# Kernel tuning notes

Hardware: AMD Instinct MI355X
Metric: run time of the kernel (lower is better)

## Reference

```python
import jax, jax.numpy as jnp
import numpy as np

STRIDES = [(2, 2), (3, 3), (4, 4)]
EPS = 1e-5


def _conv1x1(x, w, b):
    # x: [B,C,H,W], w: [O,C] -> [B,O,H,W]
    return jnp.einsum('bchw,oc->bohw', x, w) + b[None, :, None, None]


def _stitch(x, hs, ws):
    # x: [B,dk,H,W] -> patches [B, hs*ws, dk*oh*ow]; patch index = i*ws + j matches
    # torch.stack over itertools.product(range(hs), range(ws)) of x[:,:,i::hs,j::ws]
    b, dk, H, W = x.shape
    oh, ow = H // hs, W // ws
    p = x.reshape(b, dk, oh, hs, ow, ws).transpose(0, 3, 5, 1, 2, 4)  # [B,hs,ws,dk,oh,ow]
    return p.reshape(b, hs * ws, dk * oh * ow)


def _unstitch(y, b, dk, hs, ws, oh, ow):
    # faithful to the torch permute(0,3,1,4,2,5): H is assembled as (hs, oh), W as (ws, ow)
    y = y.reshape(b, hs, ws, dk, oh, ow).transpose(0, 3, 1, 4, 2, 5)  # [B,dk,hs,oh,ws,ow]
    return y.reshape(b, dk, hs * oh, ws * ow)


def _attention(q, k, v):
    d = q.shape[-1]
    scores = jnp.einsum('bpd,bqd->bpq', q, k) / jnp.sqrt(jnp.asarray(d, q.dtype))
    p = jax.nn.softmax(scores, axis=-1)
    return jnp.einsum('bpq,bqd->bpd', p, v)


def _forward(x, wq, bq, wk, bk, wv, bv, w_out, b_out, gamma, beta):
    b, c, h, w = x.shape
    n = len(STRIDES)
    dk = c // n
    q = _conv1x1(x, wq, bq)
    k = _conv1x1(x, wk, bk)
    v = _conv1x1(x, wv, bv)
    outs = []
    for idx, (ws_, hs_) in enumerate(STRIDES):
        sl = slice(idx * dk, (idx + 1) * dk)
        oh, ow = h // hs_, w // ws_
        qp = _stitch(q[:, sl], hs_, ws_)
        kp = _stitch(k[:, sl], hs_, ws_)
        vp = _stitch(v[:, sl], hs_, ws_)
        y = _attention(qp, kp, vp)  # [B, hs*ws, dk*oh*ow]
        outs.append(_unstitch(y, b, dk, hs_, ws_, oh, ow))
    out = jnp.concatenate(outs, axis=1)  # [B,C,H,W]
    # output_linear: Conv3x3 -> BatchNorm2d (training-mode batch stats) -> LeakyReLU(0.2)
    y = jax.lax.conv_general_dilated(out, w_out, (1, 1), 'SAME',
                                     dimension_numbers=('NCHW', 'OIHW', 'NCHW'))
    y = y + b_out[None, :, None, None]
    mean = jnp.mean(y, axis=(0, 2, 3), keepdims=True)
    var = jnp.var(y, axis=(0, 2, 3), keepdims=True)
    y = (y - mean) * jax.lax.rsqrt(var + EPS)
    y = y * gamma[None, :, None, None] + beta[None, :, None, None]
    return jnp.where(y >= 0, y, 0.2 * y)


def setup_inputs() -> dict:
    key = jax.random.key(0)
    ks = jax.random.split(key, 10)
    B, C, H, W = 16, 192, 96, 96
    s = 0.02
    return {
        'x': jax.random.normal(ks[0], (B, C, H, W), jnp.float32),
        'wq': jax.random.normal(ks[1], (C, C), jnp.float32) * s,
        'bq': jnp.zeros((C,), jnp.float32),
        'wk': jax.random.normal(ks[2], (C, C), jnp.float32) * s,
        'bk': jnp.zeros((C,), jnp.float32),
        'wv': jax.random.normal(ks[3], (C, C), jnp.float32) * s,
        'bv': jnp.zeros((C,), jnp.float32),
        'w_out': jax.random.normal(ks[4], (C, C, 3, 3), jnp.float32) * s,
        'b_out': jnp.zeros((C,), jnp.float32),
        'gamma': jnp.ones((C,), jnp.float32),
        'beta': jnp.zeros((C,), jnp.float32),
    }


def reference(x, wq, bq, wk, bk, wv, bv, w_out, b_out, gamma, beta):
    return _forward(x, wq, bq, wk, bk, wv, bv, w_out, b_out, gamma, beta)
```

## Files before the change

### kernel.cpp

```cpp
#include <hip/hip_runtime.h>
#include <hip/hip_bf16.h>

#define BB 16
#define CC 192
#define HH 96
#define WWW 96
#define HWSZ 9216
#define DKC 64

typedef __hip_bfloat16 bf16;
typedef __attribute__((ext_vector_type(8))) short s8v;
typedef __attribute__((ext_vector_type(4))) float f32x4;

__device__ __forceinline__ float bf2f(unsigned short u) {
  union { unsigned int i; float f; } x; x.i = ((unsigned int)u) << 16; return x.f;
}
__device__ __forceinline__ unsigned short f2bf(float f) {
  union { __hip_bfloat16 h; unsigned short u; } c; c.h = __float2bfloat16(f); return c.u;
}

__global__ __launch_bounds__(256) void prep_w_kernel(const float* __restrict__ w_out,
                                                     unsigned short* __restrict__ wb9T) {
  int e = blockIdx.x * 256 + threadIdx.x;
  if (e >= 9 * CC * CC) return;
  int c = e % CC;
  int oc = (e / CC) % CC;
  int sh = e / (CC * CC);
  wb9T[e] = f2bf(w_out[((size_t)(oc * CC + c)) * 9 + sh]);
}

__global__ __launch_bounds__(256) void prep_wqkv_kernel(
    const float* __restrict__ wq, const float* __restrict__ wk, const float* __restrict__ wv,
    unsigned short* __restrict__ wqkv) {
  int e = blockIdx.x * 256 + threadIdx.x;
  if (e >= 3 * CC * CC) return;
  int sel = e / (CC * CC), r = e % (CC * CC);
  const float* w = sel == 0 ? wq : sel == 1 ? wk : wv;
  wqkv[e] = f2bf(w[r]);
}

__global__ __launch_bounds__(256) void xcvt_kernel(const float* __restrict__ x,
                                                   unsigned short* __restrict__ xb) {
  __shared__ float xt[CC][65];
  int b = blockIdx.x / 144, tile = blockIdx.x % 144;
  int pix0 = tile * 64;
  const float* xsrc = x + (size_t)b * CC * HWSZ + pix0;
  for (int e = threadIdx.x; e < CC * 16; e += 256) {
    int c = e >> 4, seg = e & 15;
    float4 t4 = *(const float4*)(xsrc + (size_t)c * HWSZ + seg * 4);
    xt[c][seg * 4 + 0] = t4.x; xt[c][seg * 4 + 1] = t4.y;
    xt[c][seg * 4 + 2] = t4.z; xt[c][seg * 4 + 3] = t4.w;
  }
  __syncthreads();
  unsigned short* dst = xb + ((size_t)(b * HWSZ + pix0)) * CC;
  for (int e = threadIdx.x; e < 24 * 64; e += 256) {
    int cg = e >> 6, p = e & 63;
    uint4 ov;
    unsigned short* ou = (unsigned short*)&ov;
    #pragma unroll
    for (int j = 0; j < 8; ++j) ou[j] = f2bf(xt[cg * 8 + j][p]);
    *(uint4*)(dst + (size_t)p * CC + cg * 8) = ov;
  }
}

__global__ __launch_bounds__(256) void qkv_mfma_kernel(
    const unsigned short* __restrict__ xb, const unsigned short* __restrict__ wqkv,
    const float* __restrict__ bq, const float* __restrict__ bk, const float* __restrict__ bv,
    unsigned short* __restrict__ q, unsigned short* __restrict__ k,
    unsigned short* __restrict__ v) {
  __shared__ unsigned short al[2][96 * 40];
  __shared__ unsigned short vt[48 * 224];
  const int tid = threadIdx.x;
  const int bid = (blockIdx.x & 7) * 576 + (blockIdx.x >> 3);
  const int sel = bid % 3;
  const int h = (bid / 3) % HH;
  const int b = bid / (3 * HH);
  const int lane = tid & 63, wid = tid >> 6;
  const int lr = lane & 15, hi8 = (lane >> 4) * 8, rowb = (lane >> 4) * 4;
  const int n0 = wid * 48;
  const unsigned short* xrow = xb + ((size_t)(b * HWSZ + h * WWW)) * CC;
  const unsigned short* wsel = wqkv + (size_t)sel * CC * CC;

  f32x4 acc[6][3];
  #pragma unroll
  for (int mt = 0; mt < 6; ++mt)
    #pragma unroll
    for (int nt = 0; nt < 3; ++nt) acc[mt][nt] = (f32x4){0.f, 0.f, 0.f, 0.f};

  auto loadB = [&](int ck, s8v (&dst)[3]) {
    const unsigned short* src = wsel + ck * 32 + hi8;
    #pragma unroll
    for (int nt = 0; nt < 3; ++nt)
      dst[nt] = *(const s8v*)(src + (size_t)(n0 + nt * 16 + lr) * CC);
  };

  s8v br0[3], br1[3], br2[3];
  {
    uint4 a0 = *(const uint4*)(xrow + (size_t)(tid >> 2) * CC + (tid & 3) * 8);
    uint4 a1;
    int u1 = tid + 256;
    if (u1 < 384) a1 = *(const uint4*)(xrow + (size_t)(u1 >> 2) * CC + (u1 & 3) * 8);
    loadB(0, br0); loadB(1, br1); loadB(2, br2);
    *(uint4*)(al[0] + (tid >> 2) * 40 + (tid & 3) * 8) = a0;
    if (u1 < 384) *(uint4*)(al[0] + (u1 >> 2) * 40 + (u1 & 3) * 8) = a1;
  }
  __syncthreads();

  auto qstep = [&](int ck, s8v (&slot)[3]) {
    uint4 ar0, ar1;
    int u1 = tid + 256;
    if (ck < 5) {
      ar0 = *(const uint4*)(xrow + (size_t)(tid >> 2) * CC + (ck + 1) * 32 + (tid & 3) * 8);
      if (u1 < 384)
        ar1 = *(const uint4*)(xrow + (size_t)(u1 >> 2) * CC + (ck + 1) * 32 + (u1 & 3) * 8);
    }
    const unsigned short* A = al[ck & 1];
    s8v a[6];
    #pragma unroll
    for (int mt = 0; mt < 6; ++mt)
      a[mt] = *(const s8v*)(A + (mt * 16 + lr) * 40 + hi8);
    #pragma unroll
    for (int mt = 0; mt < 6; ++mt)
      #pragma unroll
      for (int nt = 0; nt < 3; ++nt)
        acc[mt][nt] = __builtin_amdgcn_mfma_f32_16x16x32_bf16(a[mt], slot[nt], acc[mt][nt], 0, 0, 0);
    if (ck + 3 < 6) loadB(ck + 3, slot);
    if (ck < 5) {
      unsigned short* dstA = al[(ck + 1) & 1];
      *(uint4*)(dstA + (tid >> 2) * 40 + (tid & 3) * 8) = ar0;
      if (u1 < 384) *(uint4*)(dstA + (u1 >> 2) * 40 + (u1 & 3) * 8) = ar1;
    }
    __syncthreads();
  };
  qstep(0, br0); qstep(1, br1); qstep(2, br2);
  qstep(3, br0); qstep(4, br1); qstep(5, br2);

  const float* bsel = (sel == 0 ? bq : sel == 1 ? bk : bv);
  float bias[3];
  #pragma unroll
  for (int nt = 0; nt < 3; ++nt) bias[nt] = bsel[n0 + nt * 16 + lr];
  unsigned short* dst = (sel == 0 ? q : sel == 1 ? k : v) + ((size_t)(b * HWSZ + h * WWW)) * CC;
  #pragma unroll
  for (int pass = 0; pass < 2; ++pass) {
    if (pass) __syncthreads();
    #pragma unroll
    for (int mt2 = 0; mt2 < 3; ++mt2) {
      #pragma unroll
      for (int nt = 0; nt < 3; ++nt)
        #pragma unroll
        for (int i = 0; i < 4; ++i)
          vt[(mt2 * 16 + rowb + i) * 224 + n0 + nt * 16 + lr] =
              f2bf(acc[pass * 3 + mt2][nt][i] + bias[nt]);
    }
    __syncthreads();
    for (int e = tid; e < 48 * 24; e += 256) {
      int p = e % 48, cg = e / 48;
      *(uint4*)(dst + (size_t)(pass * 48 + p) * CC + cg * 8) = *(uint4*)(vt + p * 224 + cg * 8);
    }
  }
}

template <int HS, int WS, int OH, int OW, int IDX>
__global__ __launch_bounds__(256) void scores_kernel(
    const unsigned short* __restrict__ q, const unsigned short* __restrict__ k,
    float* __restrict__ scores) {
  constexpr int P = HS * WS;
  constexpr int PAIRS = P * P;
  constexpr int NB = 16;
  constexpr int NSUB = (256 / PAIRS) < 1 ? 1 : (256 / PAIRS);
  __shared__ float qt[128][P + 1];
  __shared__ float kt[128][P + 1];
  int b = blockIdx.x / NB;
  int blk = blockIdx.x % NB;
  const unsigned short* qb = q + (size_t)b * HWSZ * CC;
  const unsigned short* kb = k + (size_t)b * HWSZ * CC;
  int pr = threadIdx.x % PAIRS;
  int sub = threadIdx.x / PAIRS;
  int pi = pr / P, qi = pr % P;
  float acc = 0.f;
  for (int rs0 = blk * 2; rs0 < OH * OW; rs0 += NB * 2) {
    if (threadIdx.x < 16 * P) {
      int cg = threadIdx.x & 7;
      int t2 = threadIdx.x >> 3;
      int pp = t2 % P, rs2 = t2 / P;
      int rs = rs0 + rs2;
      int r = rs / OW, s = rs % OW;
      int i = pp / WS, j = pp % WS;
      int pixel = (r * HS + i) * WWW + s * WS + j;
      uint4 qv = *(const uint4*)(qb + (size_t)pixel * CC + IDX * 64 + cg * 8);
      uint4 kv = *(const uint4*)(kb + (size_t)pixel * CC + IDX * 64 + cg * 8);
      const unsigned short* qu = (const unsigned short*)&qv;
      const unsigned short* ku = (const unsigned short*)&kv;
      #pragma unroll
      for (int m = 0; m < 8; ++m) {
        qt[rs2 * 64 + cg * 8 + m][pp] = bf2f(qu[m]);
        kt[rs2 * 64 + cg * 8 + m][pp] = bf2f(ku[m]);
      }
    }
    __syncthreads();
    if (sub < NSUB) {
      #pragma unroll 4
      for (int pos = sub; pos < 128; pos += NSUB)
        acc += qt[pos][pi] * kt[pos][qi];
    }
    __syncthreads();
  }
  if (sub < NSUB) atomicAdd(scores + ((IDX * BB + b) * 256 + pr), acc);
}

__global__ void softmax_kernel(const float* __restrict__ scores, float* __restrict__ probs) {
  int t = threadIdx.x;
  int idx, b, p, P; float scale;
  if (t < 64)       { idx = 0; b = t >> 2;           p = t & 3;         P = 4;  scale = 1.f / 384.f; }
  else if (t < 208) { int u = t - 64;  idx = 1; b = u / 9;  p = u % 9;  P = 9;  scale = 1.f / 256.f; }
  else if (t < 464) { int u = t - 208; idx = 2; b = u >> 4; p = u & 15; P = 16; scale = 1.f / 192.f; }
  else return;
  const float* row = scores + (idx * BB + b) * 256 + p * P;
  float* orow = probs + (idx * BB + b) * 256 + p * P;
  float vals[16];
  float m = -1e30f;
  for (int i = 0; i < P; i++) { vals[i] = row[i] * scale; m = fmaxf(m, vals[i]); }
  float s = 0.f;
  for (int i = 0; i < P; i++) { vals[i] = expf(vals[i] - m); s += vals[i]; }
  float inv = 1.f / s;
  for (int i = 0; i < P; i++) orow[i] = vals[i] * inv;
}

template <int HS, int WS, int OH, int OW, int IDX>
__global__ __launch_bounds__(256) void pv_kernel(
    const unsigned short* __restrict__ v, const float* __restrict__ probs,
    unsigned short* __restrict__ attn) {
  constexpr int P = HS * WS;
  __shared__ unsigned short vl[HS * 96 * 72];
  __shared__ float pl[P * P];
  int b = blockIdx.x / OH;
  int r = blockIdx.x % OH;
  const int tid = threadIdx.x;
  for (int u = tid; u < HS * 96 * 8; u += 256) {
    int iq = u / 768, w = (u >> 3) % 96, cg = u & 7;
    *(uint4*)(vl + (iq * 96 + w) * 72 + cg * 8) =
        *(const uint4*)(v + ((size_t)(b * HWSZ + (r * HS + iq) * WWW + w)) * CC + IDX * 64 + cg * 8);
  }
  if (tid < P * P) pl[tid] = probs[(IDX * BB + b) * 256 + tid];
  __syncthreads();
  for (int u = tid; u < HS * 96 * 8; u += 256) {
    int i = u / 768, w = (u >> 3) % 96, cg = u & 7;
    int j = w / OW, s = w - j * OW;
    int p = i * WS + j;
    float acc[8];
    #pragma unroll
    for (int m = 0; m < 8; ++m) acc[m] = 0.f;
    #pragma unroll
    for (int iq = 0; iq < HS; ++iq) {
      #pragma unroll
      for (int jq = 0; jq < WS; ++jq) {
        float pw = pl[p * P + iq * WS + jq];
        s8v vv = *(const s8v*)(vl + (iq * 96 + s * WS + jq) * 72 + cg * 8);
        #pragma unroll
        for (int m = 0; m < 8; ++m) acc[m] += pw * bf2f((unsigned short)vv[m]);
      }
    }
    uint4 ov;
    ov.x = (unsigned int)f2bf(acc[0]) | ((unsigned int)f2bf(acc[1]) << 16);
    ov.y = (unsigned int)f2bf(acc[2]) | ((unsigned int)f2bf(acc[3]) << 16);
    ov.z = (unsigned int)f2bf(acc[4]) | ((unsigned int)f2bf(acc[5]) << 16);
    ov.w = (unsigned int)f2bf(acc[6]) | ((unsigned int)f2bf(acc[7]) << 16);
    *(uint4*)(attn + ((size_t)(b * HWSZ + (i * OH + r) * WWW + w)) * CC + IDX * 64 + cg * 8) = ov;
  }
}

__global__ __launch_bounds__(256) void conv_mfma_kernel(
    const unsigned short* __restrict__ attn, const unsigned short* __restrict__ wb9T,
    const float* __restrict__ b_out, unsigned short* __restrict__ ybf,
    float* __restrict__ bnsum, float* __restrict__ bnsqs) {
  __shared__ unsigned short al[2][3 * 98 * 40];
  const int tid = threadIdx.x;
  const int bid = (blockIdx.x & 7) * 192 + (blockIdx.x >> 3);
  const int h = bid % HH;
  const int b = bid / HH;
  const int lane = tid & 63, wid = tid >> 6;
  const int lr = lane & 15, hi8 = (lane >> 4) * 8, rowb = (lane >> 4) * 4;
  const int n0 = wid * 48;

  f32x4 acc[6][3];
  #pragma unroll
  for (int mt = 0; mt < 6; ++mt)
    #pragma unroll
    for (int nt = 0; nt < 3; ++nt) acc[mt][nt] = (f32x4){0.f, 0.f, 0.f, 0.f};

  uint4 aregs[5];
  auto stageA_LOAD = [&](int chunk) {
    int c0 = chunk * 32;
    #pragma unroll
    for (int i = 0; i < 5; ++i) {
      int u = tid + i * 256;
      if (u < 1176) {
        int row = u / 392, rem = u % 392, wx = rem >> 2, qq = rem & 3;
        int hr = h + row - 1, w = wx - 1;
        uint4 val = make_uint4(0u, 0u, 0u, 0u);
        if (hr >= 0 && hr < HH && w >= 0 && w < WWW)
          val = *(const uint4*)(attn + ((size_t)(b * HWSZ + hr * WWW + w)) * CC + c0 + qq * 8);
        aregs[i] = val;
      }
    }
  };
  auto stageA_WRITE = [&](int chunk) {
    unsigned short* dst = al[chunk & 1];
    #pragma unroll
    for (int i = 0; i < 5; ++i) {
      int u = tid + i * 256;
      if (u < 1176) {
        int row = u / 392, rem = u % 392, wx = rem >> 2, qq = rem & 3;
        *(uint4*)(dst + (row * 98 + wx) * 40 + qq * 8) = aregs[i];
      }
    }
  };
  auto loadB = [&](int it2, s8v (&dst)[3]) {
    int chunk = it2 / 9, sh = it2 % 9;
    const unsigned short* src = wb9T + (size_t)sh * CC * CC + chunk * 32 + hi8;
    #pragma unroll
    for (int nt = 0; nt < 3; ++nt)
      dst[nt] = *(const s8v*)(src + (size_t)(n0 + nt * 16 + lr) * CC);
  };

  s8v br0[3], br1[3], br2[3];
  stageA_LOAD(0);
  stageA_WRITE(0);
  loadB(0, br0); loadB(1, br1); loadB(2, br2);
  __syncthreads();

  auto step = [&](int it, s8v (&slot)[3]) {
    int chunk = it / 9, sh = it % 9, ky = sh / 3, kx = sh % 3;
    if (sh == 0 && chunk < 5) stageA_LOAD(chunk + 1);
    const unsigned short* A = al[chunk & 1];
    s8v a[6];
    #pragma unroll
    for (int mt = 0; mt < 6; ++mt)
      a[mt] = *(const s8v*)(A + (ky * 98 + mt * 16 + lr + kx) * 40 + hi8);
    #pragma unroll
    for (int mt = 0; mt < 6; ++mt)
      #pragma unroll
      for (int nt = 0; nt < 3; ++nt)
        acc[mt][nt] = __builtin_amdgcn_mfma_f32_16x16x32_bf16(a[mt], slot[nt], acc[mt][nt], 0, 0, 0);
    if (it + 3 < 54) loadB(it + 3, slot);
    if (sh == 7 && chunk < 5) stageA_WRITE(chunk + 1);
    if (sh == 8) __syncthreads();
  };
  for (int it3 = 0; it3 < 54; it3 += 3) {
    step(it3 + 0, br0);
    step(it3 + 1, br1);
    step(it3 + 2, br2);
  }

  float s1[3], s2[3];
  #pragma unroll
  for (int nt = 0; nt < 3; ++nt) { s1[nt] = 0.f; s2[nt] = 0.f; }
  #pragma unroll
  for (int nt = 0; nt < 3; ++nt) {
    int oc = n0 + nt * 16 + lr;
    float bias = b_out[oc];
    #pragma unroll
    for (int mt = 0; mt < 6; ++mt) {
      float v0 = acc[mt][nt][0] + bias;
      float v1 = acc[mt][nt][1] + bias;
      float v2 = acc[mt][nt][2] + bias;
      float v3 = acc[mt][nt][3] + bias;
      s1[nt] += v0 + v1 + v2 + v3;
      s2[nt] += v0 * v0 + v1 * v1 + v2 * v2 + v3 * v3;
      uint2 pk;
      pk.x = (unsigned int)f2bf(v0) | ((unsigned int)f2bf(v1) << 16);
      pk.y = (unsigned int)f2bf(v2) | ((unsigned int)f2bf(v3) << 16);
      *(uint2*)(ybf + ((size_t)(b * CC + oc)) * HWSZ + h * WWW + mt * 16 + rowb) = pk;
    }
  }
  #pragma unroll
  for (int nt = 0; nt < 3; ++nt) {
    s1[nt] += __shfl_down(s1[nt], 32);
    s1[nt] += __shfl_down(s1[nt], 16);
    s2[nt] += __shfl_down(s2[nt], 32);
    s2[nt] += __shfl_down(s2[nt], 16);
  }
  if (lane < 16) {
    #pragma unroll
    for (int nt = 0; nt < 3; ++nt) {
      atomicAdd(bnsum + n0 + nt * 16 + lane, s1[nt]);
      atomicAdd(bnsqs + n0 + nt * 16 + lane, s2[nt]);
    }
  }
}

__global__ void bnfin_kernel(const float* __restrict__ bnsum, const float* __restrict__ bnsqs,
                             const float* __restrict__ gamma, const float* __restrict__ beta,
                             float* __restrict__ scale, float* __restrict__ shift) {
  int c = threadIdx.x;
  if (c >= CC) return;
  const float n = 16.f * 9216.f;
  float mean = bnsum[c] / n;
  float var = bnsqs[c] / n - mean * mean;
  float inv = rsqrtf(var + 1e-5f);
  float sc = gamma[c] * inv;
  scale[c] = sc;
  shift[c] = beta[c] - mean * sc;
}

__global__ __launch_bounds__(256) void bnapply_kernel(const unsigned short* __restrict__ ybf,
                                                      float* __restrict__ y,
                                                      const float* __restrict__ scale,
                                                      const float* __restrict__ shift) {
  const int total8 = BB * CC * HWSZ / 8;
  for (int e = blockIdx.x * 256 + threadIdx.x; e < total8; e += gridDim.x * 256) {
    uint4 t = ((const uint4*)ybf)[e];
    const unsigned short* u = (const unsigned short*)&t;
    int oc = (e / (HWSZ / 8)) % CC;
    float sc = scale[oc], sh = shift[oc];
    float4 o0, o1;
    float w;
    w = bf2f(u[0]) * sc + sh; o0.x = w >= 0.f ? w : 0.2f * w;
    w = bf2f(u[1]) * sc + sh; o0.y = w >= 0.f ? w : 0.2f * w;
    w = bf2f(u[2]) * sc + sh; o0.z = w >= 0.f ? w : 0.2f * w;
    w = bf2f(u[3]) * sc + sh; o0.w = w >= 0.f ? w : 0.2f * w;
    w = bf2f(u[4]) * sc + sh; o1.x = w >= 0.f ? w : 0.2f * w;
    w = bf2f(u[5]) * sc + sh; o1.y = w >= 0.f ? w : 0.2f * w;
    w = bf2f(u[6]) * sc + sh; o1.z = w >= 0.f ? w : 0.2f * w;
    w = bf2f(u[7]) * sc + sh; o1.w = w >= 0.f ? w : 0.2f * w;
    ((float4*)y)[e * 2] = o0;
    ((float4*)y)[e * 2 + 1] = o1;
  }
}

extern "C" void kernel_launch(void* const* d_in, const int* in_sizes, int n_in,
                              void* d_out, int out_size, void* d_ws, size_t ws_size,
                              hipStream_t stream) {
  const float* x     = (const float*)d_in[0];
  const float* wq    = (const float*)d_in[1];
  const float* bq    = (const float*)d_in[2];
  const float* wk    = (const float*)d_in[3];
  const float* bk    = (const float*)d_in[4];
  const float* wv    = (const float*)d_in[5];
  const float* bv    = (const float*)d_in[6];
  const float* w_out = (const float*)d_in[7];
  const float* b_out = (const float*)d_in[8];
  const float* gamma = (const float*)d_in[9];
  const float* beta  = (const float*)d_in[10];

  char* ws = (char*)d_ws;
  const size_t TB = (size_t)BB * CC * HWSZ * sizeof(bf16);
  unsigned short* q    = (unsigned short*)(ws);
  unsigned short* ybf  = q;
  unsigned short* k    = (unsigned short*)(ws + TB);
  unsigned short* v    = (unsigned short*)(ws + 2 * TB);
  unsigned short* attn = (unsigned short*)(ws + 3 * TB);
  unsigned short* xb   = attn;
  unsigned short* wb9T = (unsigned short*)(ws + 4 * TB);
  unsigned short* wqkv = (unsigned short*)(ws + 4 * TB + 663552);
  float* scores = (float*)(ws + 4 * TB + 663552 + 221184);
  float* bnsum  = scores + 3 * BB * 256;
  float* bnsqs  = bnsum + CC;
  float* probs  = bnsqs + CC;
  float* scale  = probs + 3 * BB * 256;
  float* shift  = scale + CC;
  float* y = (float*)d_out;

  hipMemsetAsync(scores, 0, 49152 + 2 * CC * 4, stream);

  prep_w_kernel<<<(9 * CC * CC + 255) / 256, 256, 0, stream>>>(w_out, wb9T);
  prep_wqkv_kernel<<<(3 * CC * CC + 255) / 256, 256, 0, stream>>>(wq, wk, wv, wqkv);

  xcvt_kernel<<<BB * 144, 256, 0, stream>>>(x, xb);
  qkv_mfma_kernel<<<BB * HH * 3, 256, 0, stream>>>(xb, wqkv, bq, bk, bv, q, k, v);

  scores_kernel<2, 2, 48, 48, 0><<<BB * 16, 256, 0, stream>>>(q, k, scores);
  scores_kernel<3, 3, 32, 32, 1><<<BB * 16, 256, 0, stream>>>(q, k, scores);
  scores_kernel<4, 4, 24, 24, 2><<<BB * 16, 256, 0, stream>>>(q, k, scores);

  softmax_kernel<<<1, 512, 0, stream>>>(scores, probs);

  pv_kernel<2, 2, 48, 48, 0><<<BB * 48, 256, 0, stream>>>(v, probs, attn);
  pv_kernel<3, 3, 32, 32, 1><<<BB * 32, 256, 0, stream>>>(v, probs, attn);
  pv_kernel<4, 4, 24, 24, 2><<<BB * 24, 256, 0, stream>>>(v, probs, attn);

  conv_mfma_kernel<<<BB * HH, 256, 0, stream>>>(attn, wb9T, b_out, ybf, bnsum, bnsqs);

  bnfin_kernel<<<1, 256, 0, stream>>>(bnsum, bnsqs, gamma, beta, scale, shift);
  bnapply_kernel<<<2048, 256, 0, stream>>>(ybf, y, scale, shift);
}
```

Baseline: 505.4 us.

## Compute Q, K and V per block from one LDS-resident x row with A-fragment prefetch

The QKV projection now launches one block per (batch, row) instead of three. Each block loads the whole 96x192 input row into LDS once and loops over the three weight matrices, so x is read from global memory once rather than three times and the per-chunk syncs disappear. The QKV and conv kernels also double-buffer the A fragments in registers, loading the next step's LDS data before the current MFMAs. The trade-offs are a third as many blocks, more LDS per block (which lowers occupancy), and higher register pressure.

```diff
diff --git a/kernel.cpp b/kernel.cpp
--- a/kernel.cpp
+++ b/kernel.cpp
@@ -63,99 +63,91 @@
   }
 }
 
+#define VTS 232
 __global__ __launch_bounds__(256) void qkv_mfma_kernel(
     const unsigned short* __restrict__ xb, const unsigned short* __restrict__ wqkv,
     const float* __restrict__ bq, const float* __restrict__ bk, const float* __restrict__ bv,
     unsigned short* __restrict__ q, unsigned short* __restrict__ k,
     unsigned short* __restrict__ v) {
-  __shared__ unsigned short al[2][96 * 40];
-  __shared__ unsigned short vt[48 * 224];
+  __shared__ unsigned short xl[96 * 200];
+  __shared__ unsigned short vt[48 * VTS];
   const int tid = threadIdx.x;
-  const int bid = (blockIdx.x & 7) * 576 + (blockIdx.x >> 3);
-  const int sel = bid % 3;
-  const int h = (bid / 3) % HH;
-  const int b = bid / (3 * HH);
+  const int bid = (blockIdx.x & 7) * 192 + (blockIdx.x >> 3);
+  const int h = bid % HH;
+  const int b = bid / HH;
   const int lane = tid & 63, wid = tid >> 6;
   const int lr = lane & 15, hi8 = (lane >> 4) * 8, rowb = (lane >> 4) * 4;
   const int n0 = wid * 48;
   const unsigned short* xrow = xb + ((size_t)(b * HWSZ + h * WWW)) * CC;
-  const unsigned short* wsel = wqkv + (size_t)sel * CC * CC;
-
-  f32x4 acc[6][3];
+
   #pragma unroll
-  for (int mt = 0; mt < 6; ++mt)
-    #pragma unroll
-    for (int nt = 0; nt < 3; ++nt) acc[mt][nt] = (f32x4){0.f, 0.f, 0.f, 0.f};
-
-  auto loadB = [&](int ck, s8v (&dst)[3]) {
-    const unsigned short* src = wsel + ck * 32 + hi8;
-    #pragma unroll
-    for (int nt = 0; nt < 3; ++nt)
-      dst[nt] = *(const s8v*)(src + (size_t)(n0 + nt * 16 + lr) * CC);
-  };
-
-  s8v br0[3], br1[3], br2[3];
-  {
-    uint4 a0 = *(const uint4*)(xrow + (size_t)(tid >> 2) * CC + (tid & 3) * 8);
-    uint4 a1;
-    int u1 = tid + 256;
-    if (u1 < 384) a1 = *(const uint4*)(xrow + (size_t)(u1 >> 2) * CC + (u1 & 3) * 8);
+  for (int i = 0; i < 9; ++i) {
+    int u = tid + i * 256;
+    int pix = u / 24, cg = u % 24;
+    *(uint4*)(xl + pix * 200 + cg * 8) = *(const uint4*)(xrow + (size_t)pix * CC + cg * 8);
+  }
+  __syncthreads();
+
+  for (int sel = 0; sel < 3; ++sel) {
+    const unsigned short* wsel = wqkv + (size_t)sel * CC * CC;
+    f32x4 acc[6][3];
+    #pragma unroll
+    for (int mt = 0; mt < 6; ++mt)
+      #pragma unroll
+      for (int nt = 0; nt < 3; ++nt) acc[mt][nt] = (f32x4){0.f, 0.f, 0.f, 0.f};
+
+    auto loadB = [&](int ck, s8v (&dst)[3]) {
+      const unsigned short* src = wsel + ck * 32 + hi8;
+      #pragma unroll
+      for (int nt = 0; nt < 3; ++nt)
+        dst[nt] = *(const s8v*)(src + (size_t)(n0 + nt * 16 + lr) * CC);
+    };
+    auto loadA = [&](int ck, s8v (&dst)[6]) {
+      #pragma unroll
+      for (int mt = 0; mt < 6; ++mt)
+        dst[mt] = *(const s8v*)(xl + (mt * 16 + lr) * 200 + ck * 32 + hi8);
+    };
+    auto qstep = [&](int ck, s8v (&slot)[3], s8v (&acur)[6], s8v (&anxt)[6]) {
+      if (ck < 5) loadA(ck + 1, anxt);
+      #pragma unroll
+      for (int mt = 0; mt < 6; ++mt)
+        #pragma unroll
+        for (int nt = 0; nt < 3; ++nt)
+          acc[mt][nt] = __builtin_amdgcn_mfma_f32_16x16x32_bf16(acur[mt], slot[nt], acc[mt][nt], 0, 0, 0);
+      if (ck + 3 < 6) loadB(ck + 3, slot);
+    };
+
+    s8v br0[3], br1[3], br2[3], aA[6], aB[6];
     loadB(0, br0); loadB(1, br1); loadB(2, br2);
-    *(uint4*)(al[0] + (tid >> 2) * 40 + (tid & 3) * 8) = a0;
-    if (u1 < 384) *(uint4*)(al[0] + (u1 >> 2) * 40 + (u1 & 3) * 8) = a1;
-  }
-  __syncthreads();
-
-  auto qstep = [&](int ck, s8v (&slot)[3]) {
-    uint4 ar0, ar1;
-    int u1 = tid + 256;
-    if (ck < 5) {
-      ar0 = *(const uint4*)(xrow + (size_t)(tid >> 2) * CC + (ck + 1) * 32 + (tid & 3) * 8);
-      if (u1 < 384)
-        ar1 = *(const uint4*)(xrow + (size_t)(u1 >> 2) * CC + (ck + 1) * 32 + (u1 & 3) * 8);
-    }
-    const unsigned short* A = al[ck & 1];
-    s8v a[6];
-    #pragma unroll
-    for (int mt = 0; mt < 6; ++mt)
-      a[mt] = *(const s8v*)(A + (mt * 16 + lr) * 40 + hi8);
-    #pragma unroll
-    for (int mt = 0; mt < 6; ++mt)
-      #pragma unroll
-      for (int nt = 0; nt < 3; ++nt)
-        acc[mt][nt] = __builtin_amdgcn_mfma_f32_16x16x32_bf16(a[mt], slot[nt], acc[mt][nt], 0, 0, 0);
-    if (ck + 3 < 6) loadB(ck + 3, slot);
-    if (ck < 5) {
-      unsigned short* dstA = al[(ck + 1) & 1];
-      *(uint4*)(dstA + (tid >> 2) * 40 + (tid & 3) * 8) = ar0;
-      if (u1 < 384) *(uint4*)(dstA + (u1 >> 2) * 40 + (u1 & 3) * 8) = ar1;
-    }
-    __syncthreads();
-  };
-  qstep(0, br0); qstep(1, br1); qstep(2, br2);
-  qstep(3, br0); qstep(4, br1); qstep(5, br2);
-
-  const float* bsel = (sel == 0 ? bq : sel == 1 ? bk : bv);
-  float bias[3];
-  #pragma unroll
-  for (int nt = 0; nt < 3; ++nt) bias[nt] = bsel[n0 + nt * 16 + lr];
-  unsigned short* dst = (sel == 0 ? q : sel == 1 ? k : v) + ((size_t)(b * HWSZ + h * WWW)) * CC;
-  #pragma unroll
-  for (int pass = 0; pass < 2; ++pass) {
-    if (pass) __syncthreads();
-    #pragma unroll
-    for (int mt2 = 0; mt2 < 3; ++mt2) {
-      #pragma unroll
-      for (int nt = 0; nt < 3; ++nt)
+    loadA(0, aA);
+    qstep(0, br0, aA, aB);
+    qstep(1, br1, aB, aA);
+    qstep(2, br2, aA, aB);
+    qstep(3, br0, aB, aA);
+    qstep(4, br1, aA, aB);
+    qstep(5, br2, aB, aA);
+
+    const float* bsel = (sel == 0 ? bq : sel == 1 ? bk : bv);
+    float bias[3];
+    #pragma unroll
+    for (int nt = 0; nt < 3; ++nt) bias[nt] = bsel[n0 + nt * 16 + lr];
+    unsigned short* dst = (sel == 0 ? q : sel == 1 ? k : v) + ((size_t)(b * HWSZ + h * WWW)) * CC;
+    #pragma unroll
+    for (int pass = 0; pass < 2; ++pass) {
+      __syncthreads();
+      #pragma unroll
+      for (int mt2 = 0; mt2 < 3; ++mt2)
         #pragma unroll
-        for (int i = 0; i < 4; ++i)
-          vt[(mt2 * 16 + rowb + i) * 224 + n0 + nt * 16 + lr] =
-              f2bf(acc[pass * 3 + mt2][nt][i] + bias[nt]);
-    }
-    __syncthreads();
-    for (int e = tid; e < 48 * 24; e += 256) {
-      int p = e % 48, cg = e / 48;
-      *(uint4*)(dst + (size_t)(pass * 48 + p) * CC + cg * 8) = *(uint4*)(vt + p * 224 + cg * 8);
+        for (int nt = 0; nt < 3; ++nt)
+          #pragma unroll
+          for (int i = 0; i < 4; ++i)
+            vt[(mt2 * 16 + rowb + i) * VTS + n0 + nt * 16 + lr] =
+                f2bf(acc[pass * 3 + mt2][nt][i] + bias[nt]);
+      __syncthreads();
+      for (int e = tid; e < 48 * 24; e += 256) {
+        int p = e % 48, cg = e / 48;
+        *(uint4*)(dst + (size_t)(pass * 48 + p) * CC + cg * 8) = *(uint4*)(vt + p * VTS + cg * 8);
+      }
     }
   }
 }
@@ -322,69 +314,71 @@
     for (int nt = 0; nt < 3; ++nt)
       dst[nt] = *(const s8v*)(src + (size_t)(n0 + nt * 16 + lr) * CC);
   };
-
-  s8v br0[3], br1[3], br2[3];
+  auto loadA = [&](int it2, s8v (&dst)[6]) {
+    int chunk = it2 / 9, sh = it2 % 9, ky = sh / 3, kx = sh % 3;
+    const unsigned short* A = al[chunk & 1];
+    #pragma unroll
+    for (int mt = 0; mt < 6; ++mt)
+      dst[mt] = *(const s8v*)(A + (ky * 98 + mt * 16 + lr + kx) * 40 + hi8);
+  };
+
+  s8v br0[3], br1[3], br2[3], aA[6], aB[6];
   stageA_LOAD(0);
   stageA_WRITE(0);
   loadB(0, br0); loadB(1, br1); loadB(2, br2);
   __syncthreads();
-
-  auto step = [&](int it, s8v (&slot)[3]) {
-    int chunk = it / 9, sh = it % 9, ky = sh / 3, kx = sh % 3;
+  loadA(0, aA);
+
+  auto cstep = [&](int it, s8v (&slot)[3], s8v (&acur)[6], s8v (&anxt)[6]) {
+    int chunk = it / 9, sh = it % 9;
     if (sh == 0 && chunk < 5) stageA_LOAD(chunk + 1);
-    const unsigned short* A = al[chunk & 1];
-    s8v a[6];
+    if (it < 53 && sh < 8) loadA(it + 1, anxt);
     #pragma unroll
     for (int mt = 0; mt < 6; ++mt)
-      a[mt] = *(const s8v*)(A + (ky * 98 + mt * 16 + lr + kx) * 40 + hi8);
-    #pragma unroll
-    for (int mt = 0; mt < 6; ++mt)
       #pragma unroll
       for (int nt = 0; nt < 3; ++nt)
-        acc[mt][nt] = __builtin_amdgcn_mfma_f32_16x16x32_bf16(a[mt], slot[nt], acc[mt][nt], 0, 0, 0);
+        acc[mt][nt] = __builtin_amdgcn_mfma_f32_16x16x32_bf16(acur[mt], slot[nt], acc[mt][nt], 0, 0, 0);
     if (it + 3 < 54) loadB(it + 3, slot);
     if (sh == 7 && chunk < 5) stageA_WRITE(chunk + 1);
-    if (sh == 8) __syncthreads();
+    if (sh == 8) {
+      __syncthreads();
+      if (it < 53) loadA(it + 1, anxt);
+    }
   };
-  for (int it3 = 0; it3 < 54; it3 += 3) {
-    step(it3 + 0, br0);
-    step(it3 + 1, br1);
-    step(it3 + 2, br2);
-  }
-
-  float s1[3], s2[3];
-  #pragma unroll
-  for (int nt = 0; nt < 3; ++nt) { s1[nt] = 0.f; s2[nt] = 0.f; }
+  for (int base = 0; base < 54; base += 6) {
+    cstep(base + 0, br0, aA, aB);
+    cstep(base + 1, br1, aB, aA);
+    cstep(base + 2, br2, aA, aB);
+    cstep(base + 3, br0, aB, aA);
+    cstep(base + 4, br1, aA, aB);
+    cstep(base + 5, br2, aB, aA);
+  }
+
   #pragma unroll
   for (int nt = 0; nt < 3; ++nt) {
     int oc = n0 + nt * 16 + lr;
     float bias = b_out[oc];
+    float s1 = 0.f, s2 = 0.f;
     #pragma unroll
     for (int mt = 0; mt < 6; ++mt) {
       float v0 = acc[mt][nt][0] + bias;
       float v1 = acc[mt][nt][1] + bias;
       float v2 = acc[mt][nt][2] + bias;
       float v3 = acc[mt][nt][3] + bias;
-      s1[nt] += v0 + v1 + v2 + v3;
-      s2[nt] += v0 * v0 + v1 * v1 + v2 * v2 + v3 * v3;
+      s1 += v0 + v1 + v2 + v3;
+      s2 += v0 * v0 + v1 * v1 + v2 * v2 + v3 * v3;
       uint2 pk;
       pk.x = (unsigned int)f2bf(v0) | ((unsigned int)f2bf(v1) << 16);
       pk.y = (unsigned int)f2bf(v2) | ((unsigned int)f2bf(v3) << 16);
       *(uint2*)(ybf + ((size_t)(b * CC + oc)) * HWSZ + h * WWW + mt * 16 + rowb) = pk;
     }
-  }
-  #pragma unroll
-  for (int nt = 0; nt < 3; ++nt) {
-    s1[nt] += __shfl_down(s1[nt], 32);
-    s1[nt] += __shfl_down(s1[nt], 16);
-    s2[nt] += __shfl_down(s2[nt], 32);
-    s2[nt] += __shfl_down(s2[nt], 16);
-  }
-  if (lane < 16) {
-    #pragma unroll
-    for (int nt = 0; nt < 3; ++nt) {
-      atomicAdd(bnsum + n0 + nt * 16 + lane, s1[nt]);
-      atomicAdd(bnsqs + n0 + nt * 16 + lane, s2[nt]);
+    s1 += __shfl_down(s1, 32);
+    s1 += __shfl_down(s1, 16);
+    s2 += __shfl_down(s2, 32);
+    s2 += __shfl_down(s2, 16);
+    if (lane < 16) {
+      atomicAdd(bnsum + oc, s1);
+      atomicAdd(bnsqs + oc, s2);
     }
   }
 }
@@ -467,7 +461,7 @@
   prep_wqkv_kernel<<<(3 * CC * CC + 255) / 256, 256, 0, stream>>>(wq, wk, wv, wqkv);
 
   xcvt_kernel<<<BB * 144, 256, 0, stream>>>(x, xb);
-  qkv_mfma_kernel<<<BB * HH * 3, 256, 0, stream>>>(xb, wqkv, bq, bk, bv, q, k, v);
+  qkv_mfma_kernel<<<BB * HH, 256, 0, stream>>>(xb, wqkv, bq, bk, bv, q, k, v);
 
   scores_kernel<2, 2, 48, 48, 0><<<BB * 16, 256, 0, stream>>>(q, k, scores);
   scores_kernel<3, 3, 32, 32, 1><<<BB * 16, 256, 0, stream>>>(q, k, scores);
```

Result: slower. 541.9 us (+7.2%).
